# Optimization experiments

Measured on AMD Instinct MI355X. Metric: run time of the kernel, lower is better.

Reference implementation:

```python
import jax, jax.numpy as jnp
import numpy as np


def setup_inputs() -> dict:
    key = jax.random.key(0)
    k1, k2 = jax.random.split(key)
    B, N, C, H, W = 16, 10000, 3, 32, 32
    x = jax.random.normal(k1, (B, C, H, W), dtype=jnp.float32)
    images = jax.random.normal(k2, (N, C, H, W), dtype=jnp.float32)
    # sval = schedule(t) in (0,1); bt^2 = sval, at = sqrt(1 - sval)
    sval = jnp.asarray(0.5, dtype=jnp.float32)
    return {"x": x, "images": images, "sval": sval}


def reference(x, images, sval):
    # Original math: pwise = x[:,None] - at*images[None]
    #   weights = softmax(-||pwise||^2 / (2 bt^2), over N)
    #   out = -sum_n weights_n * pwise_n / bt^2
    # We decompose ||x - at*img||^2 = ||x||^2 - 2 at x.img + at^2 ||img||^2
    # (GEMM form) and use sum_n w_n (x - at*img_n) = x - at*(w @ imgs),
    # avoiding the [B,N,C,H,W] intermediate. Identical math.
    bt2 = sval                      # bt^2 = schedule(t)
    at = jnp.sqrt(1.0 - sval)       # at = sqrt(1 - schedule(t))
    B = x.shape[0]
    N = images.shape[0]
    xf = x.reshape(B, -1)           # [B, D]
    imf = images.reshape(N, -1)     # [N, D]
    x_sq = jnp.sum(xf * xf, axis=-1)        # [B]
    i_sq = jnp.sum(imf * imf, axis=-1)      # [N]
    cross = xf @ imf.T                      # [B, N]  (main GEMM)
    weight_args = -(x_sq[:, None] - 2.0 * at * cross
                    + (at * at) * i_sq[None, :]) / (2.0 * bt2)
    weights = jax.nn.softmax(weight_args, axis=1)   # [B, N]
    mix = weights @ imf                             # [B, D]
    out = -(xf - at * mix) / bt2                    # [B, D]
    return out.reshape(x.shape)
```

## Files before the change

kernel.cpp:

```cpp
#include <hip/hip_runtime.h>
#include <math.h>

#define BB 16
#define NN 10000
#define DD 3072
#define SEL_CUT 40.0f

__global__ __launch_bounds__(256) void k1_args(
    const float* __restrict__ x, const float* __restrict__ images,
    const float* __restrict__ svalp, float* __restrict__ args)
{
  const int t = threadIdx.x;
  const int lane = t & 63;
  const int wave = t >> 6;
  const int n0 = blockIdx.x * 16 + wave * 4;

  float dotv[4][BB];
  float isq[4];
#pragma unroll
  for (int r = 0; r < 4; ++r) {
    isq[r] = 0.f;
#pragma unroll
    for (int b = 0; b < BB; ++b) dotv[r][b] = 0.f;
  }

#pragma unroll 1
  for (int c = 0; c < DD / 256; ++c) {
    const int dg = c * 256 + (lane << 2);
    float4 im[4];
#pragma unroll
    for (int r = 0; r < 4; ++r)
      im[r] = *(const float4*)&images[(size_t)(n0 + r) * DD + dg];
#pragma unroll
    for (int r = 0; r < 4; ++r)
      isq[r] += im[r].x * im[r].x + im[r].y * im[r].y +
                im[r].z * im[r].z + im[r].w * im[r].w;
#pragma unroll
    for (int b = 0; b < BB; ++b) {
      float4 xv = *(const float4*)&x[b * DD + dg];
#pragma unroll
      for (int r = 0; r < 4; ++r)
        dotv[r][b] += im[r].x * xv.x + im[r].y * xv.y +
                      im[r].z * xv.z + im[r].w * xv.w;
    }
  }

#pragma unroll
  for (int r = 0; r < 4; ++r) {
#pragma unroll
    for (int b = 0; b < BB; ++b) {
      float v = dotv[r][b];
#pragma unroll
      for (int m = 32; m >= 1; m >>= 1) v += __shfl_xor(v, m, 64);
      dotv[r][b] = v;
    }
    float v = isq[r];
#pragma unroll
    for (int m = 32; m >= 1; m >>= 1) v += __shfl_xor(v, m, 64);
    isq[r] = v;
  }

  const float sval = *svalp;
  const float at = sqrtf(1.f - sval);
  const float c1 = at / sval;
  const float c2 = (1.f - sval) / (2.f * sval);

  if (lane < BB) {
#pragma unroll
    for (int r = 0; r < 4; ++r) {
      float dv = dotv[r][0];
#pragma unroll
      for (int b = 1; b < BB; ++b)
        if (lane == b) dv = dotv[r][b];
      args[lane * NN + (n0 + r)] = c1 * dv - c2 * isq[r];
    }
  }
}

__global__ __launch_bounds__(1024) void k2_select(
    const float* __restrict__ args, int* __restrict__ cnt,
    int* __restrict__ idx, float* __restrict__ wv)
{
  __shared__ float red[16];
  __shared__ float mshared, lshared;
  const int b = blockIdx.x;
  const int t = threadIdx.x;
  const int lane = t & 63, wave = t >> 6;
  if (t == 0) cnt[b] = 0;
  const float* row = args + b * NN;

  float mx = -INFINITY;
  for (int n = t; n < NN; n += 1024) mx = fmaxf(mx, row[n]);
#pragma unroll
  for (int m = 32; m >= 1; m >>= 1) mx = fmaxf(mx, __shfl_xor(mx, m, 64));
  if (lane == 0) red[wave] = mx;
  __syncthreads();
  if (wave == 0) {
    float v = (lane < 16) ? red[lane] : -INFINITY;
#pragma unroll
    for (int m = 8; m >= 1; m >>= 1) v = fmaxf(v, __shfl_xor(v, m, 64));
    if (lane == 0) mshared = v;
  }
  __syncthreads();
  mx = mshared;

  float s = 0.f;
  for (int n = t; n < NN; n += 1024) s += __expf(row[n] - mx);
#pragma unroll
  for (int m = 32; m >= 1; m >>= 1) s += __shfl_xor(s, m, 64);
  if (lane == 0) red[wave] = s;
  __syncthreads();
  if (wave == 0) {
    float v = (lane < 16) ? red[lane] : 0.f;
#pragma unroll
    for (int m = 8; m >= 1; m >>= 1) v += __shfl_xor(v, m, 64);
    if (lane == 0) lshared = v;
  }
  __syncthreads();
  const float invl = 1.f / lshared;

  for (int n = t; n < NN; n += 1024) {
    float a = row[n];
    if (a > mx - SEL_CUT) {
      int k = atomicAdd(&cnt[b], 1);
      idx[b * NN + k] = n;
      wv[b * NN + k] = __expf(a - mx) * invl;
    }
  }
}

__global__ __launch_bounds__(256) void k3_sparse(
    const float* __restrict__ images, const float* __restrict__ x,
    const float* __restrict__ svalp, const int* __restrict__ cnt,
    const int* __restrict__ idx, const float* __restrict__ wv,
    float* __restrict__ out)
{
  const int b = blockIdx.y;
  const int d0 = blockIdx.x * 1024 + (threadIdx.x << 2);
  const int c = cnt[b];

  float4 acc = make_float4(0.f, 0.f, 0.f, 0.f);
  for (int j = 0; j < c; ++j) {
    int n = idx[b * NN + j];
    float w = wv[b * NN + j];
    float4 im = *(const float4*)&images[(size_t)n * DD + d0];
    acc.x += w * im.x; acc.y += w * im.y;
    acc.z += w * im.z; acc.w += w * im.w;
  }

  const float sval = *svalp;
  const float at = sqrtf(1.f - sval);
  const float inv_bt2 = 1.f / sval;
  float4 xv = *(const float4*)&x[b * DD + d0];
  float4 o;
  o.x = (at * acc.x - xv.x) * inv_bt2;
  o.y = (at * acc.y - xv.y) * inv_bt2;
  o.z = (at * acc.z - xv.z) * inv_bt2;
  o.w = (at * acc.w - xv.w) * inv_bt2;
  *(float4*)&out[b * DD + d0] = o;
}

extern "C" void kernel_launch(void* const* d_in, const int* in_sizes, int n_in,
                              void* d_out, int out_size, void* d_ws, size_t ws_size,
                              hipStream_t stream) {
  const float* x      = (const float*)d_in[0];
  const float* images = (const float*)d_in[1];
  const float* sval   = (const float*)d_in[2];
  float* out = (float*)d_out;
  float* ws  = (float*)d_ws;

  float* args = ws;
  int*   cnt  = (int*)(ws + 160000);
  int*   idx  = (int*)(ws + 160032);
  float* wv   = ws + 320032;

  hipLaunchKernelGGL(k1_args, dim3(625), dim3(256), 0, stream,
                     x, images, sval, args);
  hipLaunchKernelGGL(k2_select, dim3(16), dim3(1024), 0, stream,
                     args, cnt, idx, wv);
  hipLaunchKernelGGL(k3_sparse, dim3(3, 16), dim3(256), 0, stream,
                     images, x, sval, cnt, idx, wv, out);
}
```

Baseline: 227.5 us.

## Split k1 reduction over D into two halves and stage x in LDS

The distance kernel now splits the D dimension into two segments across a second grid dimension, which doubles the number of blocks from 625 to 1250 for better CU occupancy. It writes partial dot products and squared norms, and the select kernel combines them and applies the scaling. Each k-chunk of x is staged in shared memory instead of being re-read from global/L2 by every wave. The select kernel also keeps the computed args in registers rather than re-reading the row three times. In exchange it adds extra partial-result traffic and two barriers per chunk.

```diff
diff --git a/kernel.cpp b/kernel.cpp
--- a/kernel.cpp
+++ b/kernel.cpp
@@ -4,16 +4,22 @@
 #define BB 16
 #define NN 10000
 #define DD 3072
+#define DSPLIT 2
+#define DSEG (DD / DSPLIT)
+#define DC 256
 #define SEL_CUT 40.0f
 
-__global__ __launch_bounds__(256) void k1_args(
+__global__ __launch_bounds__(256) void k1_partial(
     const float* __restrict__ x, const float* __restrict__ images,
-    const float* __restrict__ svalp, float* __restrict__ args)
+    float* __restrict__ pd, float* __restrict__ pisq)
 {
+  __shared__ float xs[BB * DC];
   const int t = threadIdx.x;
   const int lane = t & 63;
   const int wave = t >> 6;
+  const int q = blockIdx.y;
   const int n0 = blockIdx.x * 16 + wave * 4;
+  const int dbase = q * DSEG;
 
   float dotv[4][BB];
   float isq[4];
@@ -25,8 +31,19 @@
   }
 
 #pragma unroll 1
-  for (int c = 0; c < DD / 256; ++c) {
-    const int dg = c * 256 + (lane << 2);
+  for (int c = 0; c < DSEG / DC; ++c) {
+    __syncthreads();
+#pragma unroll
+    for (int k = 0; k < 4; ++k) {
+      int f = t + 256 * k;
+      int row = f >> 6;
+      int col = (f & 63) << 2;
+      *(float4*)&xs[row * DC + col] =
+          *(const float4*)&x[row * DD + dbase + c * DC + col];
+    }
+    __syncthreads();
+
+    const int dg = dbase + c * DC + (lane << 2);
     float4 im[4];
 #pragma unroll
     for (int r = 0; r < 4; ++r)
@@ -37,7 +54,7 @@
                 im[r].z * im[r].z + im[r].w * im[r].w;
 #pragma unroll
     for (int b = 0; b < BB; ++b) {
-      float4 xv = *(const float4*)&x[b * DD + dg];
+      float4 xv = *(const float4*)&xs[b * DC + (lane << 2)];
 #pragma unroll
       for (int r = 0; r < 4; ++r)
         dotv[r][b] += im[r].x * xv.x + im[r].y * xv.y +
@@ -60,11 +77,6 @@
     isq[r] = v;
   }
 
-  const float sval = *svalp;
-  const float at = sqrtf(1.f - sval);
-  const float c1 = at / sval;
-  const float c2 = (1.f - sval) / (2.f * sval);
-
   if (lane < BB) {
 #pragma unroll
     for (int r = 0; r < 4; ++r) {
@@ -72,13 +84,21 @@
 #pragma unroll
       for (int b = 1; b < BB; ++b)
         if (lane == b) dv = dotv[r][b];
-      args[lane * NN + (n0 + r)] = c1 * dv - c2 * isq[r];
-    }
+      pd[(size_t)q * BB * NN + lane * NN + (n0 + r)] = dv;
+    }
+  }
+  if (lane < 4) {
+    float v = isq[0];
+#pragma unroll
+    for (int r = 1; r < 4; ++r)
+      if (lane == r) v = isq[r];
+    pisq[q * NN + n0 + lane] = v;
   }
 }
 
 __global__ __launch_bounds__(1024) void k2_select(
-    const float* __restrict__ args, int* __restrict__ cnt,
+    const float* __restrict__ pd, const float* __restrict__ pisq,
+    const float* __restrict__ svalp, int* __restrict__ cnt,
     int* __restrict__ idx, float* __restrict__ wv)
 {
   __shared__ float red[16];
@@ -87,10 +107,30 @@
   const int t = threadIdx.x;
   const int lane = t & 63, wave = t >> 6;
   if (t == 0) cnt[b] = 0;
-  const float* row = args + b * NN;
+
+  const float sval = *svalp;
+  const float at = sqrtf(1.f - sval);
+  const float c1 = at / sval;
+  const float c2 = (1.f - sval) / (2.f * sval);
+
+  float a[10];
+#pragma unroll
+  for (int i = 0; i < 10; ++i) {
+    int n = t + (i << 10);
+    if (n < NN) {
+      float d0 = pd[b * NN + n];
+      float d1 = pd[(size_t)BB * NN + b * NN + n];
+      float s0 = pisq[n];
+      float s1 = pisq[NN + n];
+      a[i] = c1 * (d0 + d1) - c2 * (s0 + s1);
+    } else {
+      a[i] = -INFINITY;
+    }
+  }
 
   float mx = -INFINITY;
-  for (int n = t; n < NN; n += 1024) mx = fmaxf(mx, row[n]);
+#pragma unroll
+  for (int i = 0; i < 10; ++i) mx = fmaxf(mx, a[i]);
 #pragma unroll
   for (int m = 32; m >= 1; m >>= 1) mx = fmaxf(mx, __shfl_xor(mx, m, 64));
   if (lane == 0) red[wave] = mx;
@@ -105,7 +145,8 @@
   mx = mshared;
 
   float s = 0.f;
-  for (int n = t; n < NN; n += 1024) s += __expf(row[n] - mx);
+#pragma unroll
+  for (int i = 0; i < 10; ++i) s += __expf(a[i] - mx);
 #pragma unroll
   for (int m = 32; m >= 1; m >>= 1) s += __shfl_xor(s, m, 64);
   if (lane == 0) red[wave] = s;
@@ -119,12 +160,12 @@
   __syncthreads();
   const float invl = 1.f / lshared;
 
-  for (int n = t; n < NN; n += 1024) {
-    float a = row[n];
-    if (a > mx - SEL_CUT) {
+#pragma unroll
+  for (int i = 0; i < 10; ++i) {
+    if (a[i] > mx - SEL_CUT) {
       int k = atomicAdd(&cnt[b], 1);
-      idx[b * NN + k] = n;
-      wv[b * NN + k] = __expf(a - mx) * invl;
+      idx[b * NN + k] = t + (i << 10);
+      wv[b * NN + k] = __expf(a[i] - mx) * invl;
     }
   }
 }
@@ -169,15 +210,16 @@
   float* out = (float*)d_out;
   float* ws  = (float*)d_ws;
 
-  float* args = ws;
-  int*   cnt  = (int*)(ws + 160000);
-  int*   idx  = (int*)(ws + 160032);
-  float* wv   = ws + 320032;
-
-  hipLaunchKernelGGL(k1_args, dim3(625), dim3(256), 0, stream,
-                     x, images, sval, args);
+  float* pd   = ws;
+  float* pisq = ws + 320000;
+  int*   cnt  = (int*)(ws + 340000);
+  int*   idx  = (int*)(ws + 340032);
+  float* wv   = ws + 500032;
+
+  hipLaunchKernelGGL(k1_partial, dim3(625, DSPLIT), dim3(256), 0, stream,
+                     x, images, pd, pisq);
   hipLaunchKernelGGL(k2_select, dim3(16), dim3(1024), 0, stream,
-                     args, cnt, idx, wv);
+                     pd, pisq, sval, cnt, idx, wv);
   hipLaunchKernelGGL(k3_sparse, dim3(3, 16), dim3(256), 0, stream,
                      images, x, sval, cnt, idx, wv, out);
 }
```

Result: no change. 228.6 us (+0.5%).

## Split GEMM over D into four partial slices and use a butterfly transpose-reduce

Applied to the files above, without the earlier changes.

The first kernel now splits the 3072-long reduction into four 768-wide slices across a second grid dimension, raising the block count from 625 to 2500 so more waves are in flight. It stores partial scores to a workspace, and the select kernel sums the four partials with a float4 load and keeps them in registers instead of re-reading the row three times. The per-lane shuffle reduction of 64 accumulators is replaced by a recursive-halving exchange that needs far fewer shuffles. In exchange the intermediate buffer becomes four times larger, and the c2*isq term is now applied once per slice using each slice's partial norm, which sums to the same total.

```diff
diff --git a/kernel.cpp b/kernel.cpp
--- a/kernel.cpp
+++ b/kernel.cpp
@@ -6,27 +6,39 @@
 #define DD 3072
 #define SEL_CUT 40.0f
 
-__global__ __launch_bounds__(256) void k1_args(
+#define RSTEP(mm, cc)                                              \
+  {                                                                \
+    const bool up = (lane & (mm)) != 0;                            \
+    _Pragma("unroll")                                              \
+    for (int k = 0; k < (cc); ++k) {                               \
+      float lo = acc[k], hi = acc[k + (cc)];                       \
+      float send = up ? lo : hi;                                   \
+      float recv = __shfl_xor(send, (mm), 64);                     \
+      acc[k] = (up ? hi : lo) + recv;                              \
+    }                                                              \
+  }
+
+__global__ __launch_bounds__(256, 3) void k1_partial(
     const float* __restrict__ x, const float* __restrict__ images,
-    const float* __restrict__ svalp, float* __restrict__ args)
+    const float* __restrict__ svalp, float* __restrict__ pd)
 {
   const int t = threadIdx.x;
   const int lane = t & 63;
   const int wave = t >> 6;
   const int n0 = blockIdx.x * 16 + wave * 4;
-
-  float dotv[4][BB];
+  const int q = blockIdx.y;
+  const int d0 = q * 768;
+
+  float acc[64];
   float isq[4];
 #pragma unroll
-  for (int r = 0; r < 4; ++r) {
-    isq[r] = 0.f;
-#pragma unroll
-    for (int b = 0; b < BB; ++b) dotv[r][b] = 0.f;
-  }
+  for (int j = 0; j < 64; ++j) acc[j] = 0.f;
+#pragma unroll
+  for (int r = 0; r < 4; ++r) isq[r] = 0.f;
 
 #pragma unroll 1
-  for (int c = 0; c < DD / 256; ++c) {
-    const int dg = c * 256 + (lane << 2);
+  for (int c = 0; c < 3; ++c) {
+    const int dg = d0 + c * 256 + (lane << 2);
     float4 im[4];
 #pragma unroll
     for (int r = 0; r < 4; ++r)
@@ -40,20 +52,20 @@
       float4 xv = *(const float4*)&x[b * DD + dg];
 #pragma unroll
       for (int r = 0; r < 4; ++r)
-        dotv[r][b] += im[r].x * xv.x + im[r].y * xv.y +
-                      im[r].z * xv.z + im[r].w * xv.w;
+        acc[b * 4 + r] += im[r].x * xv.x + im[r].y * xv.y +
+                          im[r].z * xv.z + im[r].w * xv.w;
     }
   }
 
+  RSTEP(32, 32)
+  RSTEP(16, 16)
+  RSTEP(8, 8)
+  RSTEP(4, 4)
+  RSTEP(2, 2)
+  RSTEP(1, 1)
+
 #pragma unroll
   for (int r = 0; r < 4; ++r) {
-#pragma unroll
-    for (int b = 0; b < BB; ++b) {
-      float v = dotv[r][b];
-#pragma unroll
-      for (int m = 32; m >= 1; m >>= 1) v += __shfl_xor(v, m, 64);
-      dotv[r][b] = v;
-    }
     float v = isq[r];
 #pragma unroll
     for (int m = 32; m >= 1; m >>= 1) v += __shfl_xor(v, m, 64);
@@ -65,20 +77,18 @@
   const float c1 = at / sval;
   const float c2 = (1.f - sval) / (2.f * sval);
 
-  if (lane < BB) {
-#pragma unroll
-    for (int r = 0; r < 4; ++r) {
-      float dv = dotv[r][0];
-#pragma unroll
-      for (int b = 1; b < BB; ++b)
-        if (lane == b) dv = dotv[r][b];
-      args[lane * NN + (n0 + r)] = c1 * dv - c2 * isq[r];
-    }
-  }
+  const int b = lane >> 2;
+  const int r = lane & 3;
+  float myisq = isq[0];
+  if (r == 1) myisq = isq[1];
+  if (r == 2) myisq = isq[2];
+  if (r == 3) myisq = isq[3];
+
+  pd[(size_t)b * NN * 4 + (size_t)(n0 + r) * 4 + q] = c1 * acc[0] - c2 * myisq;
 }
 
 __global__ __launch_bounds__(1024) void k2_select(
-    const float* __restrict__ args, int* __restrict__ cnt,
+    const float* __restrict__ pd, int* __restrict__ cnt,
     int* __restrict__ idx, float* __restrict__ wv)
 {
   __shared__ float red[16];
@@ -87,10 +97,22 @@
   const int t = threadIdx.x;
   const int lane = t & 63, wave = t >> 6;
   if (t == 0) cnt[b] = 0;
-  const float* row = args + b * NN;
+
+  float a[10];
+#pragma unroll
+  for (int i = 0; i < 10; ++i) {
+    int n = t + (i << 10);
+    if (n < NN) {
+      float4 p = *(const float4*)&pd[(size_t)b * NN * 4 + (size_t)n * 4];
+      a[i] = (p.x + p.y) + (p.z + p.w);
+    } else {
+      a[i] = -INFINITY;
+    }
+  }
 
   float mx = -INFINITY;
-  for (int n = t; n < NN; n += 1024) mx = fmaxf(mx, row[n]);
+#pragma unroll
+  for (int i = 0; i < 10; ++i) mx = fmaxf(mx, a[i]);
 #pragma unroll
   for (int m = 32; m >= 1; m >>= 1) mx = fmaxf(mx, __shfl_xor(mx, m, 64));
   if (lane == 0) red[wave] = mx;
@@ -105,7 +127,8 @@
   mx = mshared;
 
   float s = 0.f;
-  for (int n = t; n < NN; n += 1024) s += __expf(row[n] - mx);
+#pragma unroll
+  for (int i = 0; i < 10; ++i) s += __expf(a[i] - mx);
 #pragma unroll
   for (int m = 32; m >= 1; m >>= 1) s += __shfl_xor(s, m, 64);
   if (lane == 0) red[wave] = s;
@@ -119,12 +142,12 @@
   __syncthreads();
   const float invl = 1.f / lshared;
 
-  for (int n = t; n < NN; n += 1024) {
-    float a = row[n];
-    if (a > mx - SEL_CUT) {
+#pragma unroll
+  for (int i = 0; i < 10; ++i) {
+    if (a[i] > mx - SEL_CUT) {
       int k = atomicAdd(&cnt[b], 1);
-      idx[b * NN + k] = n;
-      wv[b * NN + k] = __expf(a - mx) * invl;
+      idx[b * NN + k] = t + (i << 10);
+      wv[b * NN + k] = __expf(a[i] - mx) * invl;
     }
   }
 }
@@ -169,15 +192,15 @@
   float* out = (float*)d_out;
   float* ws  = (float*)d_ws;
 
-  float* args = ws;
-  int*   cnt  = (int*)(ws + 160000);
-  int*   idx  = (int*)(ws + 160032);
-  float* wv   = ws + 320032;
-
-  hipLaunchKernelGGL(k1_args, dim3(625), dim3(256), 0, stream,
-                     x, images, sval, args);
+  float* pd  = ws;
+  int*   cnt = (int*)(ws + 640000);
+  int*   idx = (int*)(ws + 640032);
+  float* wv  = ws + 800032;
+
+  hipLaunchKernelGGL(k1_partial, dim3(625, 4), dim3(256), 0, stream,
+                     x, images, sval, pd);
   hipLaunchKernelGGL(k2_select, dim3(16), dim3(1024), 0, stream,
-                     args, cnt, idx, wv);
+                     pd, cnt, idx, wv);
   hipLaunchKernelGGL(k3_sparse, dim3(3, 16), dim3(256), 0, stream,
                      images, x, sval, cnt, idx, wv, out);
 }
```

Result: slower. 235.9 us (+3.7%).
